# Optimization experiments

Hardware: AMD Instinct MI355X
Metric: run time of the kernel (lower is better)

The kernel has to match this reference:

```python
import jax, jax.numpy as jnp
import numpy as np

N, T, D, K = 32, 8192, 64, 64
LOG2PI = float(np.log(2.0 * np.pi))


def setup_inputs() -> dict:
    key = jax.random.key(0)
    k1, k2, k3, k4 = jax.random.split(key, 4)
    x = jax.random.normal(k1, (N, T, D), dtype=jnp.float32)
    # valid GMM params: positive weights summing to 1, positive diagonal covariances
    weights = jax.nn.softmax(jax.random.normal(k2, (K,), dtype=jnp.float32))
    means = jax.random.normal(k3, (K, D), dtype=jnp.float32)
    covars = jax.random.uniform(k4, (K, D), dtype=jnp.float32, minval=0.5, maxval=1.5)
    return {"x": x, "weights": weights, "means": means, "covars": covars}


def _posterior(x, weights, means, covars):
    # diagonal-GMM predict_proba without materializing [N,T,K,D]:
    # sum_d (x-mu)^2/c = sum x^2/c - 2 sum x*mu/c + sum mu^2/c
    inv_c = 1.0 / covars                                   # [K,D]
    quad = (jnp.einsum('ntd,kd->ntk', x * x, inv_c)
            - 2.0 * jnp.einsum('ntd,kd->ntk', x, means * inv_c)
            + jnp.sum(means * means * inv_c, axis=-1))      # [N,T,K]
    log_prob = (jnp.log(weights)
                - 0.5 * (D * LOG2PI + jnp.sum(jnp.log(covars), axis=-1) + quad))
    return jax.nn.softmax(log_prob, axis=-1)               # [N,T,K]


def reference(x, weights, means, covars):
    # p = predict_proba * weights, renormalized over K (as in the torch code)
    p = _posterior(x, weights, means, covars) * weights
    p = p / jnp.sum(p, axis=-1, keepdims=True)             # [N,T,K]

    # pooled statistics over T (einsum avoids the [N,T,K,D] intermediate)
    s0 = jnp.sum(p, axis=1)                                # [N,K]
    s1 = jnp.einsum('ntk,ntd->nkd', p, x)                  # [N,K,D]
    s2 = jnp.einsum('ntk,ntd->nkd', p, x * x)              # [N,K,D]

    sw = jnp.sqrt(weights)                                 # [K]
    v0 = (s0 - T * weights) / sw                           # [N,K]
    v1 = (s1 - means * s0[..., None]) / (sw[:, None] * jnp.sqrt(covars))
    v2 = (s2 - 2.0 * means * s1 + (means ** 2 - covars) * s0[..., None]) / (
        jnp.sqrt(jnp.float32(2.0)) * sw[:, None] * covars)

    v = jnp.concatenate([v0[..., None], v1, v2], axis=2).reshape(x.shape[0], -1)
    # power normalization then L2 normalization
    v = jnp.sign(v) * jnp.sqrt(jnp.abs(v))
    v = v / jnp.linalg.norm(v, axis=1, keepdims=True)
    return v
```

## Files before the change

kernel.cpp:

```cpp
#include <hip/hip_runtime.h>
#include <math.h>

#define N_  32
#define T_  8192
#define D_  64
#define K_  64
#define CHUNKS 24
#define TB 64
#define BATCHES_PER_N (T_ / TB)
#define STATS_PER_N (K_ + 2 * K_ * D_)
#define XSTR 72

typedef _Float16 half_t;
typedef __attribute__((ext_vector_type(8)))  _Float16 v8h;
typedef __attribute__((ext_vector_type(4)))  float    v4f;
typedef __attribute__((ext_vector_type(16))) float    v16f;

__global__ void prep_kernel(const float* __restrict__ w, const float* __restrict__ mu,
                            const float* __restrict__ cv, float* __restrict__ Ap,
                            half_t* __restrict__ WH, float* __restrict__ ssq) {
    if (blockIdx.x < 8) {
#pragma unroll
        for (int i = 0; i < 4; ++i) {
            const int e = blockIdx.x * 1024 + i * 256 + threadIdx.x;
            const int j = e & 7, l = (e >> 3) & 63, fs = e >> 9;
            const int tile = fs >> 2, s = fs & 3;
            const int kc = 16 * tile + (l & 15);
            const int f  = 32 * s + 8 * (l >> 4) + j;
            float val;
            if (f < 64) val = mu[kc * 64 + f] / cv[kc * 64 + f];
            else        val = -0.5f / cv[kc * 64 + (f - 64)];
            WH[e] = (half_t)val;
        }
    } else {
        if (threadIdx.x < 32) ssq[threadIdx.x] = 0.f;
        if (threadIdx.x < K_) {
            const int k = threadIdx.x;
            float acc = 0.f;
            for (int d = 0; d < D_; ++d) {
                const int idx = k * D_ + d;
                const float c = cv[idx], m = mu[idx];
                acc += logf(c) + m * m / c;
            }
            Ap[k] = 2.f * logf(w[k]) - 0.5f * acc;
        }
    }
}

__launch_bounds__(256, 3)
__global__ void main_kernel(const float* __restrict__ x, const float* __restrict__ Ap,
                            const half_t* __restrict__ WH, float* __restrict__ outbuf,
                            int mode) {
    __shared__ half_t Xs[TB][XSTR];
    __shared__ half_t Qs[TB][XSTR];
    __shared__ half_t Pt[K_][XSTR];
    __shared__ float  s0sh[4][64];

    const int tid  = threadIdx.x;
    const int lane = tid & 63;
    const int wv   = tid >> 6;
    const int chunk = blockIdx.x;
    const int n     = blockIdx.y;
    const int q     = lane >> 4;
    const int c0    = lane & 15;
    const int tok   = 16 * wv + c0;

    const int r3   = (3 - (n % 3)) % 3;
    const int hcnt = (chunk + 2 - r3) / 3;
    const int boff = 5 * chunk + hcnt;
    const int cnt  = 5 + ((chunk % 3) == r3 ? 1 : 0);

    v8h Wf[16];
#pragma unroll
    for (int t = 0; t < 4; ++t)
#pragma unroll
        for (int s = 0; s < 4; ++s)
            Wf[t * 4 + s] = *(const v8h*)(WH + (size_t)((t * 4 + s) * 64 + lane) * 8);

    float apv[16];
#pragma unroll
    for (int t = 0; t < 4; ++t)
#pragma unroll
        for (int r = 0; r < 4; ++r) apv[t * 4 + r] = Ap[16 * t + 4 * q + r];

    float S0loc[16];
#pragma unroll
    for (int j = 0; j < 16; ++j) S0loc[j] = 0.f;

    const int sig = wv >> 1;
    const int dh  = wv & 1;
    v16f accB[2];
#pragma unroll
    for (int m = 0; m < 2; ++m)
#pragma unroll
        for (int r = 0; r < 16; ++r) accB[m][r] = 0.f;

    const size_t xbase = ((size_t)n * T_ + (size_t)boff * TB) * (size_t)D_;
    const float* xrow0 = x + xbase + tok * 64 + 8 * q;

    float4 R[4];
    R[0] = *(const float4*)(xrow0);
    R[1] = *(const float4*)(xrow0 + 4);
    R[2] = *(const float4*)(xrow0 + 32);
    R[3] = *(const float4*)(xrow0 + 36);

#pragma unroll 1
    for (int batch = 0; batch < cnt; ++batch) {
        v8h xh0, xh1, qh0, qh1;
        {
            const float4 a = R[0], b = R[1], c = R[2], d = R[3];
            xh0[0] = (half_t)a.x; xh0[1] = (half_t)a.y; xh0[2] = (half_t)a.z; xh0[3] = (half_t)a.w;
            xh0[4] = (half_t)b.x; xh0[5] = (half_t)b.y; xh0[6] = (half_t)b.z; xh0[7] = (half_t)b.w;
            xh1[0] = (half_t)c.x; xh1[1] = (half_t)c.y; xh1[2] = (half_t)c.z; xh1[3] = (half_t)c.w;
            xh1[4] = (half_t)d.x; xh1[5] = (half_t)d.y; xh1[6] = (half_t)d.z; xh1[7] = (half_t)d.w;
            qh0[0] = (half_t)(a.x * a.x); qh0[1] = (half_t)(a.y * a.y);
            qh0[2] = (half_t)(a.z * a.z); qh0[3] = (half_t)(a.w * a.w);
            qh0[4] = (half_t)(b.x * b.x); qh0[5] = (half_t)(b.y * b.y);
            qh0[6] = (half_t)(b.z * b.z); qh0[7] = (half_t)(b.w * b.w);
            qh1[0] = (half_t)(c.x * c.x); qh1[1] = (half_t)(c.y * c.y);
            qh1[2] = (half_t)(c.z * c.z); qh1[3] = (half_t)(c.w * c.w);
            qh1[4] = (half_t)(d.x * d.x); qh1[5] = (half_t)(d.y * d.y);
            qh1[6] = (half_t)(d.z * d.z); qh1[7] = (half_t)(d.w * d.w);
            *(v8h*)&Xs[tok][8 * q]      = xh0;
            *(v8h*)&Xs[tok][32 + 8 * q] = xh1;
            *(v8h*)&Qs[tok][8 * q]      = qh0;
            *(v8h*)&Qs[tok][32 + 8 * q] = qh1;
        }

        if (batch + 1 < cnt) {
            const float* xr = xrow0 + (size_t)(batch + 1) * TB * D_;
            R[0] = *(const float4*)(xr);
            R[1] = *(const float4*)(xr + 4);
            R[2] = *(const float4*)(xr + 32);
            R[3] = *(const float4*)(xr + 36);
        }

        {
            v4f acc[4];
#pragma unroll
            for (int t = 0; t < 4; ++t) acc[t] = (v4f)(0.f);
#pragma unroll
            for (int t = 0; t < 4; ++t) {
                acc[t] = __builtin_amdgcn_mfma_f32_16x16x32_f16(Wf[t * 4 + 0], xh0, acc[t], 0, 0, 0);
                acc[t] = __builtin_amdgcn_mfma_f32_16x16x32_f16(Wf[t * 4 + 1], xh1, acc[t], 0, 0, 0);
                acc[t] = __builtin_amdgcn_mfma_f32_16x16x32_f16(Wf[t * 4 + 2], qh0, acc[t], 0, 0, 0);
                acc[t] = __builtin_amdgcn_mfma_f32_16x16x32_f16(Wf[t * 4 + 3], qh1, acc[t], 0, 0, 0);
            }
            float pv[16];
            float m = -1e30f;
#pragma unroll
            for (int t = 0; t < 4; ++t)
#pragma unroll
                for (int r = 0; r < 4; ++r) {
                    const float lg = acc[t][r] + apv[t * 4 + r];
                    pv[t * 4 + r] = lg;
                    m = fmaxf(m, lg);
                }
            m = fmaxf(m, __shfl_xor(m, 16, 64));
            m = fmaxf(m, __shfl_xor(m, 32, 64));
            float ssum = 0.f;
#pragma unroll
            for (int j = 0; j < 16; ++j) { pv[j] = __expf(pv[j] - m); ssum += pv[j]; }
            ssum += __shfl_xor(ssum, 16, 64);
            ssum += __shfl_xor(ssum, 32, 64);
            const float rs = 1.f / ssum;
#pragma unroll
            for (int j = 0; j < 16; ++j) { pv[j] *= rs; S0loc[j] += pv[j]; }
#pragma unroll
            for (int t = 0; t < 4; ++t)
#pragma unroll
                for (int r = 0; r < 4; ++r)
                    Pt[16 * t + 4 * q + r][tok] = (half_t)pv[t * 4 + r];
        }
        __syncthreads();

        {
            const half_t* Bsrc = (sig == 0) ? &Xs[0][0] : &Qs[0][0];
            const int m   = lane & 31;
            const int h   = lane >> 5;
            const int d   = 32 * dh + m;
            const half_t* Arow0 = &Pt[m][0];
            const half_t* Arow1 = &Pt[32 + m][0];
#pragma unroll
            for (int st = 0; st < 4; ++st) {
                const int tB = 16 * st + 8 * h;
                const v8h a0 = *(const v8h*)(Arow0 + tB);
                const v8h a1 = *(const v8h*)(Arow1 + tB);
                v8h bf;
#pragma unroll
                for (int j = 0; j < 8; ++j)
                    bf[j] = Bsrc[(tB + j) * XSTR + d];
                accB[0] = __builtin_amdgcn_mfma_f32_32x32x16_f16(a0, bf, accB[0], 0, 0, 0);
                accB[1] = __builtin_amdgcn_mfma_f32_32x32x16_f16(a1, bf, accB[1], 0, 0, 0);
            }
        }
        __syncthreads();
    }

#pragma unroll
    for (int j = 0; j < 16; ++j) {
        float v = S0loc[j];
        v += __shfl_xor(v, 1, 64);
        v += __shfl_xor(v, 2, 64);
        v += __shfl_xor(v, 4, 64);
        v += __shfl_xor(v, 8, 64);
        S0loc[j] = v;
    }
    if (c0 == 0) {
#pragma unroll
        for (int t = 0; t < 4; ++t)
#pragma unroll
            for (int r = 0; r < 4; ++r)
                s0sh[wv][16 * t + 4 * q + r] = S0loc[t * 4 + r];
    }
    __syncthreads();

    if (mode == 1) {
        float* dstb = outbuf + (size_t)(n * CHUNKS + chunk) * STATS_PER_N;
        if (tid < 64)
            dstb[tid] = s0sh[0][tid] + s0sh[1][tid] + s0sh[2][tid] + s0sh[3][tid];
        const int d = 32 * dh + (lane & 31);
        float* dst = dstb + 64 + sig * 4096;
#pragma unroll
        for (int mt = 0; mt < 2; ++mt)
#pragma unroll
            for (int r = 0; r < 16; ++r) {
                const int kc = 32 * mt + (r & 3) + 8 * (r >> 2) + 4 * (lane >> 5);
                dst[kc * 64 + d] = accB[mt][r];
            }
    } else {
        float* sb = outbuf + (size_t)n * STATS_PER_N;
        if (tid < 64)
            atomicAdd(&sb[tid], s0sh[0][tid] + s0sh[1][tid] + s0sh[2][tid] + s0sh[3][tid]);
        const int d = 32 * dh + (lane & 31);
        float* dst = sb + 64 + sig * 4096;
#pragma unroll
        for (int mt = 0; mt < 2; ++mt)
#pragma unroll
            for (int r = 0; r < 16; ++r) {
                const int kc = 32 * mt + (r & 3) + 8 * (r >> 2) + 4 * (lane >> 5);
                atomicAdd(&dst[kc * 64 + d], accB[mt][r]);
            }
    }
}

__global__ void reduce_pow_kernel(const float* __restrict__ partials,
                                  const float* __restrict__ w, const float* __restrict__ mu,
                                  const float* __restrict__ cv,
                                  float* __restrict__ us, float* __restrict__ ssq) {
    __shared__ float red[4];
    const int e = blockIdx.x * 256 + threadIdx.x;
    const int n = blockIdx.y;
    float u = 0.f;
    if (e < STATS_PER_N) {
        const float* base = partials + (size_t)n * CHUNKS * STATS_PER_N;
        float sv = 0.f;
#pragma unroll 8
        for (int c = 0; c < CHUNKS; ++c) sv += base[(size_t)c * STATS_PER_N + e];
        float v; int oidx;
        if (e < 64) {
            const float wv = w[e];
            v = (sv - (float)T_ * wv) * rsqrtf(wv);
            oidx = e * 129;
        } else if (e < 64 + 4096) {
            const int idx = e - 64, k = idx >> 6, d = idx & 63;
            float s0v = 0.f;
#pragma unroll 8
            for (int c = 0; c < CHUNKS; ++c) s0v += base[(size_t)c * STATS_PER_N + k];
            v = (sv - mu[idx] * s0v) * rsqrtf(w[k] * cv[idx]);
            oidx = k * 129 + 1 + d;
        } else {
            const int idx = e - 4160, k = idx >> 6, d = idx & 63;
            float s0v = 0.f, s1v = 0.f;
#pragma unroll 4
            for (int c = 0; c < CHUNKS; ++c) {
                s0v += base[(size_t)c * STATS_PER_N + k];
                s1v += base[(size_t)c * STATS_PER_N + 64 + idx];
            }
            const float m_ = mu[idx], c_ = cv[idx];
            v = (sv - 2.f * m_ * s1v + (m_ * m_ - c_) * s0v) * (rsqrtf(2.f * w[k]) / c_);
            oidx = k * 129 + 65 + d;
        }
        u = (v >= 0.f) ? sqrtf(v) : -sqrtf(-v);
        us[(size_t)n * STATS_PER_N + oidx] = u;
    }
    float ss = u * u;
#pragma unroll
    for (int off = 32; off > 0; off >>= 1) ss += __shfl_xor(ss, off, 64);
    if ((threadIdx.x & 63) == 0) red[threadIdx.x >> 6] = ss;
    __syncthreads();
    if (threadIdx.x == 0)
        atomicAdd(&ssq[n], red[0] + red[1] + red[2] + red[3]);
}

__global__ void scale_kernel(const float* __restrict__ us, const float* __restrict__ ssq,
                             float* __restrict__ out) {
    const int e = blockIdx.x * 256 + threadIdx.x;
    const int n = blockIdx.y;
    if (e < STATS_PER_N)
        out[(size_t)n * STATS_PER_N + e] = us[(size_t)n * STATS_PER_N + e] * rsqrtf(ssq[n]);
}

__global__ void fin_kernel(const float* __restrict__ w, const float* __restrict__ mu,
                           const float* __restrict__ cv, const float* __restrict__ stats,
                           float* __restrict__ out) {
    __shared__ float us[STATS_PER_N];
    __shared__ float red[4];
    const int n   = blockIdx.x;
    const int tid = threadIdx.x;
    const float* sb = stats + (size_t)n * STATS_PER_N;

    float ss = 0.f;
    if (tid < 64) {
        const float wv = w[tid];
        const float v = (sb[tid] - (float)T_ * wv) * rsqrtf(wv);
        const float u = (v >= 0.f) ? sqrtf(v) : -sqrtf(-v);
        us[tid * 129] = u;
        ss = fmaf(u, u, ss);
    }
#pragma unroll 1
    for (int i = 0; i < 16; ++i) {
        const int idx = i * 256 + tid;
        const int k = idx >> 6, d = idx & 63;
        const float v = (sb[64 + idx] - mu[idx] * sb[k]) * rsqrtf(w[k] * cv[idx]);
        const float u = (v >= 0.f) ? sqrtf(v) : -sqrtf(-v);
        us[k * 129 + 1 + d] = u;
        ss = fmaf(u, u, ss);
    }
#pragma unroll 1
    for (int i = 0; i < 16; ++i) {
        const int idx = i * 256 + tid;
        const int k = idx >> 6, d = idx & 63;
        const float m_ = mu[idx], c_ = cv[idx];
        const float s1v = sb[64 + idx], s2v = sb[64 + 4096 + idx];
        const float v = (s2v - 2.f * m_ * s1v + (m_ * m_ - c_) * sb[k]) *
                        (rsqrtf(2.f * w[k]) / c_);
        const float u = (v >= 0.f) ? sqrtf(v) : -sqrtf(-v);
        us[k * 129 + 65 + d] = u;
        ss = fmaf(u, u, ss);
    }
#pragma unroll
    for (int off = 32; off > 0; off >>= 1) ss += __shfl_xor(ss, off, 64);
    if ((tid & 63) == 0) red[tid >> 6] = ss;
    __syncthreads();
    const float tot = red[0] + red[1] + red[2] + red[3];
    const float rn = rsqrtf(tot);
    for (int e = tid; e < STATS_PER_N; e += 256)
        out[(size_t)n * STATS_PER_N + e] = us[e] * rn;
}

extern "C" void kernel_launch(void* const* d_in, const int* in_sizes, int n_in,
                              void* d_out, int out_size, void* d_ws, size_t ws_size,
                              hipStream_t stream) {
    const float* x  = (const float*)d_in[0];
    const float* w  = (const float*)d_in[1];
    const float* mu = (const float*)d_in[2];
    const float* cv = (const float*)d_in[3];
    float* out = (float*)d_out;

    const size_t part_elems = (size_t)CHUNKS * N_ * STATS_PER_N;
    const size_t us_elems   = (size_t)N_ * STATS_PER_N;
    const size_t need_big = (part_elems + us_elems + 32 + K_ + (size_t)K_ * 64) * sizeof(float);

    if (ws_size >= need_big) {
        float* partials = (float*)d_ws;
        float* us  = partials + part_elems;
        float* ssq = us + us_elems;
        float* Ap  = ssq + 32;
        half_t* WH = (half_t*)(Ap + K_);

        prep_kernel<<<9, 256, 0, stream>>>(w, mu, cv, Ap, WH, ssq);
        main_kernel<<<dim3(CHUNKS, N_), 256, 0, stream>>>(x, Ap, WH, partials, 1);
        reduce_pow_kernel<<<dim3(33, N_), 256, 0, stream>>>(partials, w, mu, cv, us, ssq);
        scale_kernel<<<dim3(33, N_), 256, 0, stream>>>(us, ssq, out);
    } else {
        float* stats = (float*)d_ws;
        float* ssq = stats + us_elems;
        float* Ap  = ssq + 32;
        half_t* WH = (half_t*)(Ap + K_);

        hipMemsetAsync(stats, 0, us_elems * sizeof(float), stream);
        prep_kernel<<<9, 256, 0, stream>>>(w, mu, cv, Ap, WH, ssq);
        main_kernel<<<dim3(CHUNKS, N_), 256, 0, stream>>>(x, Ap, WH, stats, 0);
        fin_kernel<<<N_, 256, 0, stream>>>(w, mu, cv, stats, out);
    }
}
```

Baseline: 148.2 us.

## Fuse scale into reduce kernel via last-block counter and vectorize partial reduction

Removes the separate scale_kernel launch. The last block to finish for each batch row, detected with an atomic counter and thread fences, now applies the L2 normalization. The reduce kernel also processes four stats per thread with float4 loads, so its grid shrinks from 33 to 9 blocks per row. This saves a launch and a pass over global memory, at the cost of serializing the final scaling in one block per row and relying on the fence-based counter being correct.

```diff
diff --git a/kernel.cpp b/kernel.cpp
--- a/kernel.cpp
+++ b/kernel.cpp
@@ -7,7 +7,6 @@
 #define K_  64
 #define CHUNKS 24
 #define TB 64
-#define BATCHES_PER_N (T_ / TB)
 #define STATS_PER_N (K_ + 2 * K_ * D_)
 #define XSTR 72
 
@@ -18,7 +17,8 @@
 
 __global__ void prep_kernel(const float* __restrict__ w, const float* __restrict__ mu,
                             const float* __restrict__ cv, float* __restrict__ Ap,
-                            half_t* __restrict__ WH, float* __restrict__ ssq) {
+                            half_t* __restrict__ WH, float* __restrict__ ssq,
+                            int* __restrict__ cnt) {
     if (blockIdx.x < 8) {
 #pragma unroll
         for (int i = 0; i < 4; ++i) {
@@ -33,7 +33,7 @@
             WH[e] = (half_t)val;
         }
     } else {
-        if (threadIdx.x < 32) ssq[threadIdx.x] = 0.f;
+        if (threadIdx.x < 32) { ssq[threadIdx.x] = 0.f; cnt[threadIdx.x] = 0; }
         if (threadIdx.x < K_) {
             const int k = threadIdx.x;
             float acc = 0.f;
@@ -247,58 +247,86 @@
 __global__ void reduce_pow_kernel(const float* __restrict__ partials,
                                   const float* __restrict__ w, const float* __restrict__ mu,
                                   const float* __restrict__ cv,
-                                  float* __restrict__ us, float* __restrict__ ssq) {
+                                  float* __restrict__ us, float* __restrict__ ssq,
+                                  int* __restrict__ cnt, float* __restrict__ out) {
     __shared__ float red[4];
-    const int e = blockIdx.x * 256 + threadIdx.x;
-    const int n = blockIdx.y;
-    float u = 0.f;
-    if (e < STATS_PER_N) {
+    __shared__ float rss;
+    __shared__ int   lastf;
+    const int n  = blockIdx.y;
+    const int e4 = blockIdx.x * 256 + threadIdx.x;
+    const int e  = e4 * 4;
+    float ssl = 0.f;
+    if (e4 < STATS_PER_N / 4) {
         const float* base = partials + (size_t)n * CHUNKS * STATS_PER_N;
-        float sv = 0.f;
-#pragma unroll 8
-        for (int c = 0; c < CHUNKS; ++c) sv += base[(size_t)c * STATS_PER_N + e];
-        float v; int oidx;
+        v4f sv = {0.f, 0.f, 0.f, 0.f};
+#pragma unroll 6
+        for (int c = 0; c < CHUNKS; ++c)
+            sv += *(const v4f*)(base + (size_t)c * STATS_PER_N + e);
+        float u[4];
         if (e < 64) {
-            const float wv = w[e];
-            v = (sv - (float)T_ * wv) * rsqrtf(wv);
-            oidx = e * 129;
+#pragma unroll
+            for (int j = 0; j < 4; ++j) {
+                const float wv = w[e + j];
+                const float v = (sv[j] - (float)T_ * wv) * rsqrtf(wv);
+                u[j] = (v >= 0.f) ? sqrtf(v) : -sqrtf(-v);
+                us[(size_t)n * STATS_PER_N + (e + j) * 129] = u[j];
+            }
         } else if (e < 64 + 4096) {
-            const int idx = e - 64, k = idx >> 6, d = idx & 63;
+            const int idx = e - 64, k = idx >> 6, d0 = idx & 63;
             float s0v = 0.f;
-#pragma unroll 8
+#pragma unroll 6
             for (int c = 0; c < CHUNKS; ++c) s0v += base[(size_t)c * STATS_PER_N + k];
-            v = (sv - mu[idx] * s0v) * rsqrtf(w[k] * cv[idx]);
-            oidx = k * 129 + 1 + d;
+#pragma unroll
+            for (int j = 0; j < 4; ++j) {
+                const float v = (sv[j] - mu[idx + j] * s0v) * rsqrtf(w[k] * cv[idx + j]);
+                u[j] = (v >= 0.f) ? sqrtf(v) : -sqrtf(-v);
+                us[(size_t)n * STATS_PER_N + k * 129 + 1 + d0 + j] = u[j];
+            }
         } else {
-            const int idx = e - 4160, k = idx >> 6, d = idx & 63;
-            float s0v = 0.f, s1v = 0.f;
+            const int idx = e - 4160, k = idx >> 6, d0 = idx & 63;
+            float s0v = 0.f;
+            v4f  s1v = {0.f, 0.f, 0.f, 0.f};
 #pragma unroll 4
             for (int c = 0; c < CHUNKS; ++c) {
                 s0v += base[(size_t)c * STATS_PER_N + k];
-                s1v += base[(size_t)c * STATS_PER_N + 64 + idx];
-            }
-            const float m_ = mu[idx], c_ = cv[idx];
-            v = (sv - 2.f * m_ * s1v + (m_ * m_ - c_) * s0v) * (rsqrtf(2.f * w[k]) / c_);
-            oidx = k * 129 + 65 + d;
-        }
-        u = (v >= 0.f) ? sqrtf(v) : -sqrtf(-v);
-        us[(size_t)n * STATS_PER_N + oidx] = u;
-    }
-    float ss = u * u;
-#pragma unroll
-    for (int off = 32; off > 0; off >>= 1) ss += __shfl_xor(ss, off, 64);
-    if ((threadIdx.x & 63) == 0) red[threadIdx.x >> 6] = ss;
+                s1v += *(const v4f*)(base + (size_t)c * STATS_PER_N + 64 + idx);
+            }
+            const float rwk = rsqrtf(2.f * w[k]);
+#pragma unroll
+            for (int j = 0; j < 4; ++j) {
+                const float m_ = mu[idx + j], c_ = cv[idx + j];
+                const float v = (sv[j] - 2.f * m_ * s1v[j] + (m_ * m_ - c_) * s0v) * (rwk / c_);
+                u[j] = (v >= 0.f) ? sqrtf(v) : -sqrtf(-v);
+                us[(size_t)n * STATS_PER_N + k * 129 + 65 + d0 + j] = u[j];
+            }
+        }
+        ssl = u[0] * u[0] + u[1] * u[1] + u[2] * u[2] + u[3] * u[3];
+    }
+#pragma unroll
+    for (int off = 32; off > 0; off >>= 1) ssl += __shfl_xor(ssl, off, 64);
+    if ((threadIdx.x & 63) == 0) red[threadIdx.x >> 6] = ssl;
     __syncthreads();
-    if (threadIdx.x == 0)
+    if (threadIdx.x == 0) {
         atomicAdd(&ssq[n], red[0] + red[1] + red[2] + red[3]);
-}
-
-__global__ void scale_kernel(const float* __restrict__ us, const float* __restrict__ ssq,
-                             float* __restrict__ out) {
-    const int e = blockIdx.x * 256 + threadIdx.x;
-    const int n = blockIdx.y;
-    if (e < STATS_PER_N)
-        out[(size_t)n * STATS_PER_N + e] = us[(size_t)n * STATS_PER_N + e] * rsqrtf(ssq[n]);
+        __threadfence();
+        const int old = atomicAdd(&cnt[n], 1);
+        lastf = (old == (int)gridDim.x - 1);
+        if (lastf) {
+            __threadfence();
+            rss = rsqrtf(atomicAdd(&ssq[n], 0.f));
+        }
+    }
+    __syncthreads();
+    if (lastf) {
+        const float rs = rss;
+        const float* ub = us + (size_t)n * STATS_PER_N;
+        float* ob = out + (size_t)n * STATS_PER_N;
+        for (int i = threadIdx.x; i < STATS_PER_N / 4; i += 256) {
+            v4f uv = *(const v4f*)(ub + 4 * i);
+            uv *= rs;
+            *(v4f*)(ob + 4 * i) = uv;
+        }
+    }
 }
 
 __global__ void fin_kernel(const float* __restrict__ w, const float* __restrict__ mu,
@@ -360,27 +388,28 @@
 
     const size_t part_elems = (size_t)CHUNKS * N_ * STATS_PER_N;
     const size_t us_elems   = (size_t)N_ * STATS_PER_N;
-    const size_t need_big = (part_elems + us_elems + 32 + K_ + (size_t)K_ * 64) * sizeof(float);
+    const size_t need_big = (part_elems + us_elems + 32 + 32 + K_ + (size_t)K_ * 64) * sizeof(float);
 
     if (ws_size >= need_big) {
         float* partials = (float*)d_ws;
         float* us  = partials + part_elems;
         float* ssq = us + us_elems;
-        float* Ap  = ssq + 32;
+        int*   cnt = (int*)(ssq + 32);
+        float* Ap  = (float*)(cnt + 32);
         half_t* WH = (half_t*)(Ap + K_);
 
-        prep_kernel<<<9, 256, 0, stream>>>(w, mu, cv, Ap, WH, ssq);
+        prep_kernel<<<9, 256, 0, stream>>>(w, mu, cv, Ap, WH, ssq, cnt);
         main_kernel<<<dim3(CHUNKS, N_), 256, 0, stream>>>(x, Ap, WH, partials, 1);
-        reduce_pow_kernel<<<dim3(33, N_), 256, 0, stream>>>(partials, w, mu, cv, us, ssq);
-        scale_kernel<<<dim3(33, N_), 256, 0, stream>>>(us, ssq, out);
+        reduce_pow_kernel<<<dim3(9, N_), 256, 0, stream>>>(partials, w, mu, cv, us, ssq, cnt, out);
     } else {
         float* stats = (float*)d_ws;
         float* ssq = stats + us_elems;
-        float* Ap  = ssq + 32;
+        int*   cnt = (int*)(ssq + 32);
+        float* Ap  = (float*)(cnt + 32);
         half_t* WH = (half_t*)(Ap + K_);
 
         hipMemsetAsync(stats, 0, us_elems * sizeof(float), stream);
-        prep_kernel<<<9, 256, 0, stream>>>(w, mu, cv, Ap, WH, ssq);
+        prep_kernel<<<9, 256, 0, stream>>>(w, mu, cv, Ap, WH, ssq, cnt);
         main_kernel<<<dim3(CHUNKS, N_), 256, 0, stream>>>(x, Ap, WH, stats, 0);
         fin_kernel<<<N_, 256, 0, stream>>>(w, mu, cv, stats, out);
     }
```

Result: slower. 155.9 us (+5.2%).

## Use atomic-accumulation path always and fold stats zeroing into prep kernel

Applied to the files above, without the earlier changes.

Removes the large-workspace path that wrote per-chunk partials and reduced them in two extra kernels, so the atomicAdd accumulation plus fused fin_kernel path always runs. The memset of the stats buffer is folded into extra blocks of prep_kernel, cutting one launch. This trades partial-buffer write/read traffic and two launches for global atomic contention in main_kernel.

```diff
diff --git a/kernel.cpp b/kernel.cpp
--- a/kernel.cpp
+++ b/kernel.cpp
@@ -7,9 +7,10 @@
 #define K_  64
 #define CHUNKS 24
 #define TB 64
-#define BATCHES_PER_N (T_ / TB)
 #define STATS_PER_N (K_ + 2 * K_ * D_)
 #define XSTR 72
+#define STATS_TOTAL (N_ * STATS_PER_N)
+#define STATS_F4    (STATS_TOTAL / 4)
 
 typedef _Float16 half_t;
 typedef __attribute__((ext_vector_type(8)))  _Float16 v8h;
@@ -18,7 +19,7 @@
 
 __global__ void prep_kernel(const float* __restrict__ w, const float* __restrict__ mu,
                             const float* __restrict__ cv, float* __restrict__ Ap,
-                            half_t* __restrict__ WH, float* __restrict__ ssq) {
+                            half_t* __restrict__ WH, float* __restrict__ stats) {
     if (blockIdx.x < 8) {
 #pragma unroll
         for (int i = 0; i < 4; ++i) {
@@ -32,8 +33,7 @@
             else        val = -0.5f / cv[kc * 64 + (f - 64)];
             WH[e] = (half_t)val;
         }
-    } else {
-        if (threadIdx.x < 32) ssq[threadIdx.x] = 0.f;
+    } else if (blockIdx.x == 8) {
         if (threadIdx.x < K_) {
             const int k = threadIdx.x;
             float acc = 0.f;
@@ -43,6 +43,14 @@
                 acc += logf(c) + m * m / c;
             }
             Ap[k] = 2.f * logf(w[k]) - 0.5f * acc;
+        }
+    } else {
+        const int b = blockIdx.x - 9;
+        float4 z; z.x = z.y = z.z = z.w = 0.f;
+#pragma unroll
+        for (int i = 0; i < 8; ++i) {
+            const int idx = (b * 8 + i) * 256 + threadIdx.x;
+            if (idx < STATS_F4) ((float4*)stats)[idx] = z;
         }
     }
 }
@@ -244,63 +252,6 @@
     }
 }
 
-__global__ void reduce_pow_kernel(const float* __restrict__ partials,
-                                  const float* __restrict__ w, const float* __restrict__ mu,
-                                  const float* __restrict__ cv,
-                                  float* __restrict__ us, float* __restrict__ ssq) {
-    __shared__ float red[4];
-    const int e = blockIdx.x * 256 + threadIdx.x;
-    const int n = blockIdx.y;
-    float u = 0.f;
-    if (e < STATS_PER_N) {
-        const float* base = partials + (size_t)n * CHUNKS * STATS_PER_N;
-        float sv = 0.f;
-#pragma unroll 8
-        for (int c = 0; c < CHUNKS; ++c) sv += base[(size_t)c * STATS_PER_N + e];
-        float v; int oidx;
-        if (e < 64) {
-            const float wv = w[e];
-            v = (sv - (float)T_ * wv) * rsqrtf(wv);
-            oidx = e * 129;
-        } else if (e < 64 + 4096) {
-            const int idx = e - 64, k = idx >> 6, d = idx & 63;
-            float s0v = 0.f;
-#pragma unroll 8
-            for (int c = 0; c < CHUNKS; ++c) s0v += base[(size_t)c * STATS_PER_N + k];
-            v = (sv - mu[idx] * s0v) * rsqrtf(w[k] * cv[idx]);
-            oidx = k * 129 + 1 + d;
-        } else {
-            const int idx = e - 4160, k = idx >> 6, d = idx & 63;
-            float s0v = 0.f, s1v = 0.f;
-#pragma unroll 4
-            for (int c = 0; c < CHUNKS; ++c) {
-                s0v += base[(size_t)c * STATS_PER_N + k];
-                s1v += base[(size_t)c * STATS_PER_N + 64 + idx];
-            }
-            const float m_ = mu[idx], c_ = cv[idx];
-            v = (sv - 2.f * m_ * s1v + (m_ * m_ - c_) * s0v) * (rsqrtf(2.f * w[k]) / c_);
-            oidx = k * 129 + 65 + d;
-        }
-        u = (v >= 0.f) ? sqrtf(v) : -sqrtf(-v);
-        us[(size_t)n * STATS_PER_N + oidx] = u;
-    }
-    float ss = u * u;
-#pragma unroll
-    for (int off = 32; off > 0; off >>= 1) ss += __shfl_xor(ss, off, 64);
-    if ((threadIdx.x & 63) == 0) red[threadIdx.x >> 6] = ss;
-    __syncthreads();
-    if (threadIdx.x == 0)
-        atomicAdd(&ssq[n], red[0] + red[1] + red[2] + red[3]);
-}
-
-__global__ void scale_kernel(const float* __restrict__ us, const float* __restrict__ ssq,
-                             float* __restrict__ out) {
-    const int e = blockIdx.x * 256 + threadIdx.x;
-    const int n = blockIdx.y;
-    if (e < STATS_PER_N)
-        out[(size_t)n * STATS_PER_N + e] = us[(size_t)n * STATS_PER_N + e] * rsqrtf(ssq[n]);
-}
-
 __global__ void fin_kernel(const float* __restrict__ w, const float* __restrict__ mu,
                            const float* __restrict__ cv, const float* __restrict__ stats,
                            float* __restrict__ out) {
@@ -358,30 +309,11 @@
     const float* cv = (const float*)d_in[3];
     float* out = (float*)d_out;
 
-    const size_t part_elems = (size_t)CHUNKS * N_ * STATS_PER_N;
-    const size_t us_elems   = (size_t)N_ * STATS_PER_N;
-    const size_t need_big = (part_elems + us_elems + 32 + K_ + (size_t)K_ * 64) * sizeof(float);
-
-    if (ws_size >= need_big) {
-        float* partials = (float*)d_ws;
-        float* us  = partials + part_elems;
-        float* ssq = us + us_elems;
-        float* Ap  = ssq + 32;
-        half_t* WH = (half_t*)(Ap + K_);
-
-        prep_kernel<<<9, 256, 0, stream>>>(w, mu, cv, Ap, WH, ssq);
-        main_kernel<<<dim3(CHUNKS, N_), 256, 0, stream>>>(x, Ap, WH, partials, 1);
-        reduce_pow_kernel<<<dim3(33, N_), 256, 0, stream>>>(partials, w, mu, cv, us, ssq);
-        scale_kernel<<<dim3(33, N_), 256, 0, stream>>>(us, ssq, out);
-    } else {
-        float* stats = (float*)d_ws;
-        float* ssq = stats + us_elems;
-        float* Ap  = ssq + 32;
-        half_t* WH = (half_t*)(Ap + K_);
-
-        hipMemsetAsync(stats, 0, us_elems * sizeof(float), stream);
-        prep_kernel<<<9, 256, 0, stream>>>(w, mu, cv, Ap, WH, ssq);
-        main_kernel<<<dim3(CHUNKS, N_), 256, 0, stream>>>(x, Ap, WH, stats, 0);
-        fin_kernel<<<N_, 256, 0, stream>>>(w, mu, cv, stats, out);
-    }
+    float* stats = (float*)d_ws;
+    float* Ap    = stats + STATS_TOTAL;
+    half_t* WH   = (half_t*)(Ap + K_);
+
+    prep_kernel<<<42, 256, 0, stream>>>(w, mu, cv, Ap, WH, stats);
+    main_kernel<<<dim3(CHUNKS, N_), 256, 0, stream>>>(x, Ap, WH, stats, 0);
+    fin_kernel<<<N_, 256, 0, stream>>>(w, mu, cv, stats, out);
 }
```

New measurement: 156.0 us. 5.3% more time.
